# Optimization experiments

Hardware: AMD Instinct MI355X
Metric: run time of the kernel (lower is better)

Reference implementation:

```python
import jax, jax.numpy as jnp
import numpy as np

V, E, H, L, B, T = 50257, 1024, 16, 8, 2, 2048
HD = E // H  # head_dim = 64
FF = 4 * E
EPS = 1e-5


def setup_inputs() -> dict:
    key = jax.random.key(0)
    ks = jax.random.split(key, 12)
    s = 0.02  # init std as in _init_weights
    return {
        "idx": jax.random.randint(ks[0], (B, T), 0, V, dtype=jnp.int64) if jax.config.jax_enable_x64 else jax.random.randint(ks[0], (B, T), 0, V, dtype=jnp.int32),
        "targets": jax.random.randint(ks[1], (B, T), 0, V, dtype=jnp.int32),
        "wte": jax.random.normal(ks[2], (V, E), jnp.float32) * s,
        "wpe": jax.random.normal(ks[3], (T, E), jnp.float32) * s,
        "qkv_w": jax.random.normal(ks[4], (L, E, 3 * E), jnp.float32) * s,
        "proj_w": jax.random.normal(ks[5], (L, E, E), jnp.float32) * s,
        "proj_b": jnp.zeros((L, E), jnp.float32),
        "ln1_g": jnp.ones((L, E), jnp.float32),
        "ln1_b": jnp.zeros((L, E), jnp.float32),
        "ln2_g": jnp.ones((L, E), jnp.float32),
        "ln2_b": jnp.zeros((L, E), jnp.float32),
        "fc1_w": jax.random.normal(ks[6], (L, E, FF), jnp.float32) * s,
        "fc1_b": jnp.zeros((L, FF), jnp.float32),
        "fc2_w": jax.random.normal(ks[7], (L, FF, E), jnp.float32) * s,
        "fc2_b": jnp.zeros((L, E), jnp.float32),
        "lnf_g": jnp.ones((E,), jnp.float32),
        "lnf_b": jnp.zeros((E,), jnp.float32),
    }


def _layer_norm(x, g, b):
    mean = x.mean(-1, keepdims=True)
    var = ((x - mean) ** 2).mean(-1, keepdims=True)  # unbiased=False
    return g * (x - mean) / jnp.sqrt(var + EPS) + b


def _gpt_forward(idx, targets, wte, wpe, qkv_w, proj_w, proj_b,
                 ln1_g, ln1_b, ln2_g, ln2_b, fc1_w, fc1_b, fc2_w, fc2_b,
                 lnf_g, lnf_b):
    Bq, Tq = idx.shape
    x = wte[idx] + wpe[:Tq][None, :, :]  # [B,T,E]
    causal = jnp.tril(jnp.ones((Tq, Tq), bool))  # [T,T]
    scale = 1.0 / np.sqrt(HD)

    def block(x, p):
        (qw, pw, pb, g1, b1, g2, b2, f1w, f1b, f2w, f2b) = p
        h = _layer_norm(x, g1, b1)
        qkv = h @ qw  # [B,T,3E]
        qkv = qkv.reshape(Bq, Tq, 3, H, HD).transpose(2, 0, 3, 1, 4)  # [3,B,H,T,HD]
        q, k, v = qkv[0], qkv[1], qkv[2]
        att = jnp.einsum('bhqd,bhkd->bhqk', q, k) * scale
        att = jnp.where(causal[None, None], att, -jnp.inf)
        att = jax.nn.softmax(att, axis=-1)  # dropout=0.0 -> identity
        y = jnp.einsum('bhqk,bhkd->bhqd', att, v)
        y = y.transpose(0, 2, 1, 3).reshape(Bq, Tq, E)
        x = x + y @ pw + pb
        h = _layer_norm(x, g2, b2)
        h = jax.nn.gelu(h @ f1w + f1b, approximate=False)  # torch nn.GELU = exact erf
        x = x + h @ f2w + f2b
        return x, None

    params = (qkv_w, proj_w, proj_b, ln1_g, ln1_b, ln2_g, ln2_b,
              fc1_w, fc1_b, fc2_w, fc2_b)
    x, _ = jax.lax.scan(block, x, params)
    x = _layer_norm(x, lnf_g, lnf_b)
    logits = x @ wte.T  # tied lm_head, [B,T,V]
    logp = jax.nn.log_softmax(logits, axis=-1)
    nll = -jnp.take_along_axis(logp, targets[..., None], axis=-1)[..., 0]
    loss = nll.mean()
    return logits, loss


def reference(idx, targets, wte, wpe, qkv_w, proj_w, proj_b,
              ln1_g, ln1_b, ln2_g, ln2_b, fc1_w, fc1_b, fc2_w, fc2_b,
              lnf_g, lnf_b):
    return _gpt_forward(idx, targets, wte, wpe, qkv_w, proj_w, proj_b,
                        ln1_g, ln1_b, ln2_g, ln2_b, fc1_w, fc1_b, fc2_w, fc2_b,
                        lnf_g, lnf_b)
```

## Files before the change

### kernel.cpp

```cpp
#include <hip/hip_runtime.h>
#include <math.h>

constexpr int Vv = 50257;
constexpr int Ee = 1024;
constexpr int Hh = 16;
constexpr int Ll = 8;
constexpr int Bb = 2;
constexpr int Tt = 2048;
constexpr int HDh = 64;
constexpr int FFf = 4096;
constexpr int BT = Bb * Tt;

typedef __attribute__((ext_vector_type(8))) short bf16x8;
typedef __attribute__((ext_vector_type(4))) float f32x4;

__device__ __forceinline__ short f2b(float f) {
    union { float f; unsigned u; } c; c.f = f;
    unsigned u = c.u + 0x7fffu + ((c.u >> 16) & 1u);
    return (short)(u >> 16);
}

__device__ __forceinline__ void g2l16(void* lds, const void* g) {
    __builtin_amdgcn_global_load_lds(
        (const __attribute__((address_space(1))) void*)g,
        (__attribute__((address_space(3))) void*)lds, 16, 0, 0);
}

__device__ __forceinline__ float gelu_exact(float v) {
    return 0.5f * v * (1.0f + erff(v * 0.70710678118654752f));
}

__global__ __launch_bounds__(256) void k_embed(const int* __restrict__ idx,
                                               const float* __restrict__ wte,
                                               const float* __restrict__ wpe,
                                               float* __restrict__ x) {
    const int row = blockIdx.x;
    const int t = row % Tt;
    const int tok = idx[row];
    const int c = threadIdx.x * 4;
    const float4 a = *(const float4*)(wte + (size_t)tok * Ee + c);
    const float4 b = *(const float4*)(wpe + (size_t)t * Ee + c);
    *(float4*)(x + (size_t)row * Ee + c) =
        make_float4(a.x + b.x, a.y + b.y, a.z + b.z, a.w + b.w);
}

__global__ __launch_bounds__(256) void k_ln(const float* __restrict__ x,
                                            const float* __restrict__ g,
                                            const float* __restrict__ b,
                                            short* __restrict__ out) {
    const int row = blockIdx.x;
    const int tid = threadIdx.x;
    const float4 v = *(const float4*)(x + (size_t)row * Ee + tid * 4);
    float s  = v.x + v.y + v.z + v.w;
    float ss = v.x * v.x + v.y * v.y + v.z * v.z + v.w * v.w;
#pragma unroll
    for (int off = 32; off; off >>= 1) {
        s  += __shfl_down(s, off);
        ss += __shfl_down(ss, off);
    }
    __shared__ float red[8];
    const int wid = tid >> 6, lane = tid & 63;
    if (lane == 0) { red[wid] = s; red[4 + wid] = ss; }
    __syncthreads();
    const float S  = red[0] + red[1] + red[2] + red[3];
    const float SS = red[4] + red[5] + red[6] + red[7];
    const float mean = S * (1.f / Ee);
    const float var  = SS * (1.f / Ee) - mean * mean;
    const float inv  = rsqrtf(var + 1e-5f);
    const float4 gg = *(const float4*)(g + tid * 4);
    const float4 bb = *(const float4*)(b + tid * 4);
    short4 o;
    o.x = f2b((v.x - mean) * inv * gg.x + bb.x);
    o.y = f2b((v.y - mean) * inv * gg.y + bb.y);
    o.z = f2b((v.z - mean) * inv * gg.z + bb.z);
    o.w = f2b((v.w - mean) * inv * gg.w + bb.w);
    *(short4*)(out + (size_t)row * Ee + tid * 4) = o;
}

__global__ __launch_bounds__(256) void k_wT(const float* __restrict__ w,
                                            short* __restrict__ o, int K, int N) {
    __shared__ short t[32][33];
    const int n0 = blockIdx.x * 32, k0 = blockIdx.y * 32;
    const int tid = threadIdx.x;
    {
        const int k = tid >> 3, n4 = (tid & 7) * 4;
        const float4 v = *(const float4*)(w + (size_t)(k0 + k) * N + n0 + n4);
        t[n4 + 0][k] = f2b(v.x); t[n4 + 1][k] = f2b(v.y);
        t[n4 + 2][k] = f2b(v.z); t[n4 + 3][k] = f2b(v.w);
    }
    __syncthreads();
    {
        const int n = tid >> 3, k4 = (tid & 7) * 4;
        short4 s;
        s.x = t[n][k4]; s.y = t[n][k4 + 1]; s.z = t[n][k4 + 2]; s.w = t[n][k4 + 3];
        *(short4*)(o + (size_t)(n0 + n) * K + k0 + k4) = s;
    }
}

__global__ __launch_bounds__(256) void k_vT(const short* __restrict__ qkv,
                                            short* __restrict__ vT) {
    __shared__ short t[32][33];
    const int r0 = blockIdx.x * 32;
    const int c0 = blockIdx.y * 32;
    const int tid = threadIdx.x;
    {
        const int r = tid >> 3, c4 = (tid & 7) * 4;
        const short4 v = *(const short4*)(qkv + (size_t)(r0 + r) * (3 * Ee) + 2 * Ee + c0 + c4);
        t[c4 + 0][r] = v.x; t[c4 + 1][r] = v.y;
        t[c4 + 2][r] = v.z; t[c4 + 3][r] = v.w;
    }
    __syncthreads();
    {
        const int c = tid >> 3, r4 = (tid & 7) * 4;
        short4 s;
        s.x = t[c][r4]; s.y = t[c][r4 + 1]; s.z = t[c][r4 + 2]; s.w = t[c][r4 + 3];
        *(short4*)(vT + (size_t)(c0 + c) * BT + r0 + r4) = s;
    }
}

__global__ __launch_bounds__(256) void k_cvt(const float* __restrict__ w,
                                             short* __restrict__ o, int n8) {
    const int i = blockIdx.x * 256 + threadIdx.x;
    if (i >= n8) return;
    const float4 a = ((const float4*)w)[i * 2];
    const float4 b = ((const float4*)w)[i * 2 + 1];
    bf16x8 v = {f2b(a.x), f2b(a.y), f2b(a.z), f2b(a.w),
                f2b(b.x), f2b(b.y), f2b(b.z), f2b(b.w)};
    ((bf16x8*)o)[i] = v;
}

__device__ __forceinline__ void st_c(float* C, size_t i, float v) { C[i] = v; }
__device__ __forceinline__ void st_c(short* C, size_t i, float v) { C[i] = f2b(v); }

template <int EPI, int SWZ, int BN64f, int WAVES, typename OT>
__global__ __launch_bounds__(WAVES * 64) void k_gemm(const short* __restrict__ A,
                                              const short* __restrict__ Bp,
                                              const float* __restrict__ bias,
                                              const float* __restrict__ res,
                                              OT* __restrict__ C,
                                              int M, int N, int K,
                                              float* __restrict__ pmax,
                                              float* __restrict__ psum) {
    constexpr int BM = (WAVES / 2) * 64;
    constexpr int BN = BN64f ? 64 : 128;
    constexpr int NJ = BN64f ? 2 : 4;
    constexpr int WCOL = BN64f ? 32 : 64;
    __shared__ short As[BM * 32];
    __shared__ short Bs[BN * 32];
    const int tid = threadIdx.x, w = tid >> 6, ln = tid & 63;
    int bx = blockIdx.x, by = blockIdx.y;
    if (SWZ) {
        const int nwg = gridDim.x * gridDim.y;
        const int orig = by * gridDim.x + bx;
        const int q = nwg >> 3, r = nwg & 7;
        const int xcd = orig & 7, local = orig >> 3;
        const int wgid = (xcd < r ? xcd * (q + 1) : r * (q + 1) + (xcd - r) * q) + local;
        if (SWZ == 1) { bx = wgid % gridDim.x; by = wgid / gridDim.x; }
        else          { bx = wgid / gridDim.y; by = wgid % gridDim.y; }
    }
    const int m0 = bx * BM, n0 = by * BN;
    const int wr = w >> 1, wc = w & 1;

    f32x4 zero = {0.f, 0.f, 0.f, 0.f};
    f32x4 acc[4][NJ];
#pragma unroll
    for (int i = 0; i < 4; i++)
#pragma unroll
        for (int j = 0; j < NJ; j++) acc[i][j] = zero;

    const int srow = w * 32 + (ln >> 2);
    const int scol = (ln & 3) * 8;
    const int sb   = tid >> 2;
    const int sb8  = w * 16 + (ln >> 2);
    const int br0 = min(n0 + srow, N - 1);
    const int br1 = min(n0 + srow + 16, N - 1);
    const int brs = min(n0 + sb, N - 1);
    const int br8 = min(n0 + sb8, N - 1);

    for (int k0 = 0; k0 < K; k0 += 32) {
        __syncthreads();
        g2l16(&As[(w * 32 + 0) * 32],  A + (size_t)(m0 + srow) * K + k0 + scol);
        g2l16(&As[(w * 32 + 16) * 32], A + (size_t)(m0 + srow + 16) * K + k0 + scol);
        if (BN64f) {
            g2l16(&Bs[sb * 32], Bp + (size_t)brs * K + k0 + scol);
        } else if (WAVES == 8) {
            g2l16(&Bs[(w * 16) * 32], Bp + (size_t)br8 * K + k0 + scol);
        } else {
            g2l16(&Bs[(w * 32 + 0) * 32],  Bp + (size_t)br0 * K + k0 + scol);
            g2l16(&Bs[(w * 32 + 16) * 32], Bp + (size_t)br1 * K + k0 + scol);
        }
        __syncthreads();
        bf16x8 af[4], bfv[NJ];
#pragma unroll
        for (int i = 0; i < 4; i++)
            af[i]  = *(bf16x8*)&As[(wr * 64 + i * 16 + (ln & 15)) * 32 + (ln >> 4) * 8];
#pragma unroll
        for (int j = 0; j < NJ; j++)
            bfv[j] = *(bf16x8*)&Bs[(wc * WCOL + j * 16 + (ln & 15)) * 32 + (ln >> 4) * 8];
#pragma unroll
        for (int i = 0; i < 4; i++)
#pragma unroll
            for (int j = 0; j < NJ; j++)
                acc[i][j] = __builtin_amdgcn_mfma_f32_16x16x32_bf16(
                    af[i], bfv[j], acc[i][j], 0, 0, 0);
    }

#pragma unroll
    for (int j = 0; j < NJ; j++) {
        const int gcol = n0 + wc * WCOL + j * 16 + (ln & 15);
        if (gcol < N) {
            const float bv = (EPI == 2 || EPI == 3) ? bias[gcol] : 0.f;
#pragma unroll
            for (int i = 0; i < 4; i++) {
#pragma unroll
                for (int r = 0; r < 4; r++) {
                    const int grow = m0 + wr * 64 + i * 16 + (ln >> 4) * 4 + r;
                    float v = acc[i][j][r] + bv;
                    if (EPI == 2) v = gelu_exact(v);
                    if (EPI == 3) v += res[(size_t)grow * N + gcol];
                    st_c(C, (size_t)grow * N + gcol, v);
                }
            }
        }
    }
    if (EPI == 4) {
        const size_t slot = (size_t)(by * 2 + wc) * M;
#pragma unroll
        for (int i = 0; i < 4; i++) {
#pragma unroll
            for (int r = 0; r < 4; r++) {
                const int grow = m0 + wr * 64 + i * 16 + (ln >> 4) * 4 + r;
                float vv[NJ], pm = -INFINITY;
#pragma unroll
                for (int j = 0; j < NJ; j++) {
                    const int gcol = n0 + wc * WCOL + j * 16 + (ln & 15);
                    vv[j] = (gcol < N) ? acc[i][j][r] : -INFINITY;
                    pm = fmaxf(pm, vv[j]);
                }
#pragma unroll
                for (int off = 1; off < 16; off <<= 1) pm = fmaxf(pm, __shfl_xor(pm, off));
                float ps = 0.f;
#pragma unroll
                for (int j = 0; j < NJ; j++)
                    ps += (vv[j] > -INFINITY) ? __expf(vv[j] - pm) : 0.f;
#pragma unroll
                for (int off = 1; off < 16; off <<= 1) ps += __shfl_xor(ps, off);
                if ((ln & 15) == 0) {
                    pmax[slot + grow] = pm;
                    psum[slot + grow] = ps;
                }
            }
        }
    }
}

__global__ __launch_bounds__(256) void k_attn(const short* __restrict__ qkv,
                                              const short* __restrict__ vT,
                                              short* __restrict__ y) {
    __shared__ short Kl[64][72];
    __shared__ short Vt[64][72];
    __shared__ short Pl[4][16][72];
    const int tid = threadIdx.x, w = tid >> 6, ln = tid & 63;
    const int lo = blockIdx.x;
    const int hi = (Tt / 64 - 1) - lo;
    const int h = blockIdx.y, b = blockIdx.z;
    const size_t base = ((size_t)b * Tt) * (3 * Ee) + h * HDh;
    const int q0s[2] = {lo * 64, hi * 64};

    bf16x8 qf[2][2];
#pragma unroll
    for (int s = 0; s < 2; s++) {
        const int qr = q0s[s] + w * 16 + (ln & 15);
        const short* qp = qkv + base + (size_t)qr * (3 * Ee) + (ln >> 4) * 8;
        qf[s][0] = *(const bf16x8*)(qp);
        qf[s][1] = *(const bf16x8*)(qp + 32);
    }

    f32x4 zero = {0.f, 0.f, 0.f, 0.f};
    f32x4 oc[2][4];
#pragma unroll
    for (int s = 0; s < 2; s++)
#pragma unroll
        for (int i = 0; i < 4; i++) oc[s][i] = zero;
    float mx[2][4], ls[2][4];
#pragma unroll
    for (int s = 0; s < 2; s++)
#pragma unroll
        for (int r = 0; r < 4; r++) { mx[s][r] = -INFINITY; ls[s][r] = 0.f; }

    const int nt = hi + 1;
    for (int j = 0; j < nt; j++) {
        const int kb = j * 64;
        __syncthreads();
        {
            const int r = tid >> 2, d0 = (tid & 3) * 16;
            const short* kp = qkv + base + Ee + (size_t)(kb + r) * (3 * Ee) + d0;
            *(bf16x8*)&Kl[r][d0]     = *(const bf16x8*)(kp);
            *(bf16x8*)&Kl[r][d0 + 8] = *(const bf16x8*)(kp + 8);
            const short* vp = vT + (size_t)(h * HDh + r) * BT + (size_t)b * Tt + kb + d0;
            *(bf16x8*)&Vt[r][d0]     = *(const bf16x8*)(vp);
            *(bf16x8*)&Vt[r][d0 + 8] = *(const bf16x8*)(vp + 8);
        }
        __syncthreads();

#pragma unroll
        for (int s = 1; s >= 0; s--) {
            if (s == 0 && j > lo) continue;
            f32x4 sc[4];
#pragma unroll
            for (int kcb = 0; kcb < 4; kcb++) {
                const int krow = kcb * 16 + (ln & 15);
                bf16x8 kf0 = *(bf16x8*)&Kl[krow][(ln >> 4) * 8];
                bf16x8 kf1 = *(bf16x8*)&Kl[krow][(ln >> 4) * 8 + 32];
                f32x4 ss = __builtin_amdgcn_mfma_f32_16x16x32_bf16(qf[s][0], kf0, zero, 0, 0, 0);
                sc[kcb]  = __builtin_amdgcn_mfma_f32_16x16x32_bf16(qf[s][1], kf1, ss, 0, 0, 0);
            }
            float pv[4][4];
            float tmv[4] = {-INFINITY, -INFINITY, -INFINITY, -INFINITY};
#pragma unroll
            for (int kcb = 0; kcb < 4; kcb++) {
                const int col = kb + kcb * 16 + (ln & 15);
#pragma unroll
                for (int r = 0; r < 4; r++) {
                    const int qr = q0s[s] + w * 16 + (ln >> 4) * 4 + r;
                    const float sv = (col <= qr) ? sc[kcb][r] * 0.125f : -INFINITY;
                    pv[kcb][r] = sv;
                    tmv[r] = fmaxf(tmv[r], sv);
                }
            }
#pragma unroll
            for (int off = 1; off < 16; off <<= 1)
#pragma unroll
                for (int r = 0; r < 4; r++) tmv[r] = fmaxf(tmv[r], __shfl_xor(tmv[r], off));
            float rs[4];
#pragma unroll
            for (int r = 0; r < 4; r++) {
                const float nm = fmaxf(mx[s][r], tmv[r]);
                const float alpha = __expf(mx[s][r] - nm);
                mx[s][r] = nm;
                float acc_s = 0.f;
#pragma unroll
                for (int kcb = 0; kcb < 4; kcb++) {
                    const float e = __expf(pv[kcb][r] - nm);
                    pv[kcb][r] = e;
                    acc_s += e;
                }
                rs[r] = acc_s;
                ls[s][r] *= alpha;
#pragma unroll
                for (int db = 0; db < 4; db++) oc[s][db][r] *= alpha;
            }
#pragma unroll
            for (int off = 1; off < 16; off <<= 1)
#pragma unroll
                for (int r = 0; r < 4; r++) rs[r] += __shfl_xor(rs[r], off);
#pragma unroll
            for (int r = 0; r < 4; r++) ls[s][r] += rs[r];
#pragma unroll
            for (int kcb = 0; kcb < 4; kcb++)
#pragma unroll
                for (int r = 0; r < 4; r++)
                    Pl[w][(ln >> 4) * 4 + r][kcb * 16 + (ln & 15)] = f2b(pv[kcb][r]);
            bf16x8 pf0 = *(bf16x8*)&Pl[w][ln & 15][(ln >> 4) * 8];
            bf16x8 pf1 = *(bf16x8*)&Pl[w][ln & 15][(ln >> 4) * 8 + 32];
#pragma unroll
            for (int db = 0; db < 4; db++) {
                const int drow = db * 16 + (ln & 15);
                bf16x8 vf0 = *(bf16x8*)&Vt[drow][(ln >> 4) * 8];
                bf16x8 vf1 = *(bf16x8*)&Vt[drow][(ln >> 4) * 8 + 32];
                oc[s][db] = __builtin_amdgcn_mfma_f32_16x16x32_bf16(pf0, vf0, oc[s][db], 0, 0, 0);
                oc[s][db] = __builtin_amdgcn_mfma_f32_16x16x32_bf16(pf1, vf1, oc[s][db], 0, 0, 0);
            }
        }
    }
#pragma unroll
    for (int s = 0; s < 2; s++)
#pragma unroll
        for (int r = 0; r < 4; r++) {
            const int qr = q0s[s] + w * 16 + (ln >> 4) * 4 + r;
            const float inv = 1.f / ls[s][r];
#pragma unroll
            for (int db = 0; db < 4; db++)
                y[(size_t)(b * Tt + qr) * Ee + h * HDh + db * 16 + (ln & 15)] =
                    f2b(oc[s][db][r] * inv);
        }
}

__global__ __launch_bounds__(256) void k_loss_fin(const float* __restrict__ pmax,
                                                  const float* __restrict__ psum,
                                                  const float* __restrict__ logits,
                                                  const int* __restrict__ targets,
                                                  float* __restrict__ rnll, int nt2) {
    const int row = blockIdx.x * 256 + threadIdx.x;
    float M = -INFINITY, S = 0.f;
    for (int i = 0; i < nt2; i++) {
        const float pm = pmax[(size_t)i * BT + row];
        const float ps = psum[(size_t)i * BT + row];
        const float nm = fmaxf(M, pm);
        S = S * __expf(M - nm) + ps * __expf(pm - nm);
        M = nm;
    }
    rnll[row] = (M + logf(S)) - logits[(size_t)row * Vv + targets[row]];
}

__global__ __launch_bounds__(256) void k_loss_final(const float* __restrict__ rnll,
                                                    float* __restrict__ loss) {
    const int tid = threadIdx.x;
    float s = 0.f;
    for (int i = tid; i < BT; i += 256) s += rnll[i];
#pragma unroll
    for (int off = 32; off; off >>= 1) s += __shfl_xor(s, off);
    __shared__ float red[4];
    if ((tid & 63) == 0) red[tid >> 6] = s;
    __syncthreads();
    if (tid == 0) loss[0] = (red[0] + red[1] + red[2] + red[3]) / (float)BT;
}

extern "C" void kernel_launch(void* const* d_in, const int* in_sizes, int n_in,
                              void* d_out, int out_size, void* d_ws, size_t ws_size,
                              hipStream_t stream) {
    const int*   idx     = (const int*)d_in[0];
    const int*   targets = (const int*)d_in[1];
    const float* wte     = (const float*)d_in[2];
    const float* wpe     = (const float*)d_in[3];
    const float* qkv_w   = (const float*)d_in[4];
    const float* proj_w  = (const float*)d_in[5];
    const float* proj_b  = (const float*)d_in[6];
    const float* ln1_g   = (const float*)d_in[7];
    const float* ln1_b   = (const float*)d_in[8];
    const float* ln2_g   = (const float*)d_in[9];
    const float* ln2_b   = (const float*)d_in[10];
    const float* fc1_w   = (const float*)d_in[11];
    const float* fc1_b   = (const float*)d_in[12];
    const float* fc2_w   = (const float*)d_in[13];
    const float* fc2_b   = (const float*)d_in[14];
    const float* lnf_g   = (const float*)d_in[15];
    const float* lnf_b   = (const float*)d_in[16];

    float* logits = (float*)d_out;
    float* loss   = logits + (size_t)BT * Vv;

    constexpr int NT2 = 2 * ((Vv + 127) / 128);

    short* wteb = (short*)d_ws;
    float* x    = (float*)d_ws;
    short* qkvb = (short*)(x + (size_t)BT * Ee);
    short* y    = qkvb + (size_t)BT * 3 * Ee;
    short* h1   = y + (size_t)BT * Ee;
    short* wT   = h1 + (size_t)BT * FFf;
    short* vT   = wT + (size_t)FFf * Ee;
    const size_t OFF = (size_t)Vv * Ee * 2;
    short* h    = (short*)((char*)d_ws + OFF);
    float* rnll = (float*)(h + (size_t)BT * Ee);
    float* pmax = rnll + BT;
    float* psum = pmax + (size_t)BT * NT2;
    const size_t need = OFF + (size_t)BT * Ee * 2
                      + (BT + 2 * (size_t)BT * NT2) * sizeof(float);
    if (ws_size < need) return;

    k_embed<<<BT, 256, 0, stream>>>(idx, wte, wpe, x);
    for (int l = 0; l < Ll; l++) {
        k_ln<<<BT, 256, 0, stream>>>(x, ln1_g + (size_t)l * Ee, ln1_b + (size_t)l * Ee, h);
        k_wT<<<dim3(3 * Ee / 32, Ee / 32), 256, 0, stream>>>(
            qkv_w + (size_t)l * Ee * 3 * Ee, wT, Ee, 3 * Ee);
        k_gemm<0, 1, 0, 8, short><<<dim3(BT / 256, 3 * Ee / 128), 512, 0, stream>>>(
            h, wT, nullptr, nullptr, qkvb, BT, 3 * Ee, Ee, nullptr, nullptr);
        k_vT<<<dim3(BT / 32, Ee / 32), 256, 0, stream>>>(qkvb, vT);
        k_attn<<<dim3(Tt / 128, Hh, Bb), 256, 0, stream>>>(qkvb, vT, y);
        k_wT<<<dim3(Ee / 32, Ee / 32), 256, 0, stream>>>(
            proj_w + (size_t)l * Ee * Ee, wT, Ee, Ee);
        k_gemm<3, 1, 1, 4, float><<<dim3(BT / 128, Ee / 64), 256, 0, stream>>>(
            y, wT, proj_b + (size_t)l * Ee, x, x, BT, Ee, Ee, nullptr, nullptr);
        k_ln<<<BT, 256, 0, stream>>>(x, ln2_g + (size_t)l * Ee, ln2_b + (size_t)l * Ee, h);
        k_wT<<<dim3(FFf / 32, Ee / 32), 256, 0, stream>>>(
            fc1_w + (size_t)l * Ee * FFf, wT, Ee, FFf);
        k_gemm<2, 1, 0, 8, short><<<dim3(BT / 256, FFf / 128), 512, 0, stream>>>(
            h, wT, fc1_b + (size_t)l * FFf, nullptr, h1, BT, FFf, Ee, nullptr, nullptr);
        k_wT<<<dim3(Ee / 32, FFf / 32), 256, 0, stream>>>(
            fc2_w + (size_t)l * FFf * Ee, wT, FFf, Ee);
        k_gemm<3, 1, 1, 4, float><<<dim3(BT / 128, Ee / 64), 256, 0, stream>>>(
            h1, wT, fc2_b + (size_t)l * Ee, x, x, BT, Ee, FFf, nullptr, nullptr);
    }
    k_ln<<<BT, 256, 0, stream>>>(x, lnf_g, lnf_b, h);
    k_cvt<<<(Vv * Ee / 8 + 255) / 256, 256, 0, stream>>>(wte, wteb, Vv * Ee / 8);
    k_gemm<4, 2, 0, 8, float><<<dim3(BT / 256, (Vv + 127) / 128), 512, 0, stream>>>(
        h, wteb, nullptr, nullptr, logits, BT, Vv, Ee, pmax, psum);
    k_loss_fin<<<BT / 256, 256, 0, stream>>>(pmax, psum, logits, targets, rnll, NT2);
    k_loss_final<<<1, 256, 0, stream>>>(rnll, loss);
}
```

Baseline: 3.648 ms.

## Double-buffer GEMM LDS tiles to overlap global loads with MFMA

Splits the A and B shared-memory tiles into two buffers and issues the global-to-LDS loads for the next K step before computing on the current one. This leaves one barrier per iteration instead of two and is meant to hide global load latency behind MFMA work. It doubles LDS use per block, which may lower occupancy. Correctness depends on the async global_load_lds writes being complete at the barrier before the buffer is read; the code adds no explicit vmcnt wait.

After: 3.478 ms. -4.7%, faster.

```diff
diff --git a/kernel.cpp b/kernel.cpp
--- a/kernel.cpp
+++ b/kernel.cpp
@@ -145,8 +145,8 @@
     constexpr int BN = BN64f ? 64 : 128;
     constexpr int NJ = BN64f ? 2 : 4;
     constexpr int WCOL = BN64f ? 32 : 64;
-    __shared__ short As[BM * 32];
-    __shared__ short Bs[BN * 32];
+    __shared__ short As[2][BM * 32];
+    __shared__ short Bs[2][BN * 32];
     const int tid = threadIdx.x, w = tid >> 6, ln = tid & 63;
     int bx = blockIdx.x, by = blockIdx.y;
     if (SWZ) {
@@ -177,32 +177,43 @@
     const int brs = min(n0 + sb, N - 1);
     const int br8 = min(n0 + sb8, N - 1);
 
+    auto STAGE = [&](int buf, int k0) {
+        short* As_ = As[buf];
+        short* Bs_ = Bs[buf];
+        g2l16(&As_[(w * 32 + 0) * 32],  A + (size_t)(m0 + srow) * K + k0 + scol);
+        g2l16(&As_[(w * 32 + 16) * 32], A + (size_t)(m0 + srow + 16) * K + k0 + scol);
+        if (BN64f) {
+            g2l16(&Bs_[sb * 32], Bp + (size_t)brs * K + k0 + scol);
+        } else if (WAVES == 8) {
+            g2l16(&Bs_[(w * 16) * 32], Bp + (size_t)br8 * K + k0 + scol);
+        } else {
+            g2l16(&Bs_[(w * 32 + 0) * 32],  Bp + (size_t)br0 * K + k0 + scol);
+            g2l16(&Bs_[(w * 32 + 16) * 32], Bp + (size_t)br1 * K + k0 + scol);
+        }
+    };
+
+    int cur = 0;
+    STAGE(0, 0);
+    __syncthreads();
     for (int k0 = 0; k0 < K; k0 += 32) {
-        __syncthreads();
-        g2l16(&As[(w * 32 + 0) * 32],  A + (size_t)(m0 + srow) * K + k0 + scol);
-        g2l16(&As[(w * 32 + 16) * 32], A + (size_t)(m0 + srow + 16) * K + k0 + scol);
-        if (BN64f) {
-            g2l16(&Bs[sb * 32], Bp + (size_t)brs * K + k0 + scol);
-        } else if (WAVES == 8) {
-            g2l16(&Bs[(w * 16) * 32], Bp + (size_t)br8 * K + k0 + scol);
-        } else {
-            g2l16(&Bs[(w * 32 + 0) * 32],  Bp + (size_t)br0 * K + k0 + scol);
-            g2l16(&Bs[(w * 32 + 16) * 32], Bp + (size_t)br1 * K + k0 + scol);
-        }
-        __syncthreads();
+        if (k0 + 32 < K) STAGE(cur ^ 1, k0 + 32);
+        const short* Ar = As[cur];
+        const short* Br = Bs[cur];
         bf16x8 af[4], bfv[NJ];
 #pragma unroll
         for (int i = 0; i < 4; i++)
-            af[i]  = *(bf16x8*)&As[(wr * 64 + i * 16 + (ln & 15)) * 32 + (ln >> 4) * 8];
+            af[i]  = *(const bf16x8*)&Ar[(wr * 64 + i * 16 + (ln & 15)) * 32 + (ln >> 4) * 8];
 #pragma unroll
         for (int j = 0; j < NJ; j++)
-            bfv[j] = *(bf16x8*)&Bs[(wc * WCOL + j * 16 + (ln & 15)) * 32 + (ln >> 4) * 8];
+            bfv[j] = *(const bf16x8*)&Br[(wc * WCOL + j * 16 + (ln & 15)) * 32 + (ln >> 4) * 8];
 #pragma unroll
         for (int i = 0; i < 4; i++)
 #pragma unroll
             for (int j = 0; j < NJ; j++)
                 acc[i][j] = __builtin_amdgcn_mfma_f32_16x16x32_bf16(
                     af[i], bfv[j], acc[i][j], 0, 0, 0);
+        __syncthreads();
+        cur ^= 1;
     }
 
 #pragma unroll
```
